# Optimization experiments

Measured on AMD Instinct MI355X. Metric: run time of the kernel, lower is better.

Reference implementation:

```python
import jax, jax.numpy as jnp
import numpy as np

B, C, RN, K = 4, 128, 4096, 16
EPS = 1e-5

def _bn_relu(x, gamma, beta):
    # BatchNorm1d in training mode: batch stats over axis 0 (biased var)
    mu = jnp.mean(x, axis=0)
    var = jnp.mean(jnp.square(x - mu), axis=0)
    y = (x - mu) / jnp.sqrt(var + EPS) * gamma + beta
    return jax.nn.relu(y)

def _mlp(x, W, b, gamma, beta):
    return _bn_relu(x @ W.T + b, gamma, beta)

def _knn_idx(pts, k):
    # pts: (B, N, 3) -> (B, N, k) indices of k nearest (incl. self)
    sq = jnp.sum(pts * pts, axis=-1)  # (B, N)
    d2 = sq[:, :, None] + sq[:, None, :] - 2.0 * jnp.einsum('bnd,bmd->bnm', pts, pts)
    _, idx = jax.lax.top_k(-d2, k)
    return idx

def _group(feats, idx):
    # feats: (B, N, C), idx: (B, N, k) -> (B, N, k, C)
    return jax.vmap(lambda f, i: f[i])(feats, idx)

def setup_inputs() -> dict:
    key = jax.random.key(0)
    ks = jax.random.split(key, 16)
    def init_lin(k1, k2, out_c, in_c):
        lim = 1.0 / np.sqrt(in_c)
        W = jax.random.uniform(k1, (out_c, in_c), jnp.float32, -lim, lim)
        b = jax.random.uniform(k2, (out_c,), jnp.float32, -lim, lim)
        return W, b
    W1, b1 = init_lin(ks[0], ks[1], 64, 3)
    W2, b2 = init_lin(ks[2], ks[3], C, C + 64)
    Ww, bw = init_lin(ks[4], ks[5], K, 3)
    return {
        'F_E': jax.random.normal(ks[6], (B, C, RN), jnp.float32),
        'Q_prime': jax.random.normal(ks[7], (B, 3, RN), jnp.float32),
        'W1': W1, 'b1': b1, 'g1': jnp.ones((64,), jnp.float32), 'be1': jnp.zeros((64,), jnp.float32),
        'W2': W2, 'b2': b2, 'g2': jnp.ones((C,), jnp.float32), 'be2': jnp.zeros((C,), jnp.float32),
        'Ww': Ww, 'bw': bw, 'gw': jnp.ones((K,), jnp.float32), 'bew': jnp.zeros((K,), jnp.float32),
    }

def reference(F_E, Q_prime, W1, b1, g1, be1, W2, b2, g2, be2, Ww, bw, gw, bew):
    q = jnp.transpose(Q_prime, (0, 2, 1))   # (B, rN, 3)
    f = jnp.transpose(F_E, (0, 2, 1))       # (B, rN, C)
    idx = _knn_idx(q, K)                     # (B, rN, K)
    grouped_Q = _group(q, idx)               # (B, rN, K, 3)
    grouped_F = _group(f, idx)               # (B, rN, K, C)
    sub_Q = grouped_Q - q[:, :, None, :]     # (B, rN, K, 3)
    sub_flat = sub_Q.reshape(-1, 3)
    enc_sub = _mlp(sub_flat, W1, b1, g1, be1).reshape(B, RN, K, 64)
    concat = jnp.concatenate([grouped_F, enc_sub], axis=-1).reshape(-1, C + 64)
    enc_feat = _mlp(concat, W2, b2, g2, be2).reshape(B, RN, K, C)
    sw = _mlp(sub_flat, Ww, bw, gw, bew).reshape(B, RN, K, K)
    # einsum 'brkc,brkk->brkc' takes the diagonal of sw over its last two axes
    w_diag = jnp.diagonal(sw, axis1=2, axis2=3)  # (B, rN, K)
    weighted = jnp.sum(enc_feat * w_diag[..., None], axis=2)  # (B, rN, C)
    refined = weighted + f
    return jnp.transpose(refined, (0, 2, 1))
```

## Files before the change

kernel.cpp:

```cpp
#include <hip/hip_runtime.h>
#include <hip/hip_bf16.h>

#define BB 4
#define CC 128
#define RN 4096
#define KK 16
#define NROWS (BB*RN*KK)
#define EPSV 1e-5f

typedef __attribute__((ext_vector_type(8))) short short8;
typedef __attribute__((ext_vector_type(4))) float f32x4;

__device__ inline ushort f2bf(float f) {
    union { __hip_bfloat16 h; ushort u; } cv;
    cv.h = __float2bfloat16(f);
    return cv.u;
}

__device__ inline float readlane_f(float v, int src) {
    return __uint_as_float((uint)__builtin_amdgcn_readlane((int)__float_as_uint(v), src));
}


__global__ void k_prep(const float* __restrict__ Q, float4* __restrict__ qp,
                       const float* __restrict__ W2, ushort* __restrict__ W2b) {
    int blk = blockIdx.x;
    if (blk < 64) {
        int gid = blk * 256 + threadIdx.x;
        int b = gid >> 12, n = gid & (RN - 1);
        size_t base = (size_t)b * 3 * RN;
        float x = Q[base + n], y = Q[base + RN + n], z = Q[base + 2 * RN + n];
        qp[gid] = make_float4(x, y, z, fmaf(x, x, fmaf(y, y, z * z)));
    } else {
        int i = (blk - 64) * 256 + threadIdx.x;
        if (i < 128 * 192) W2b[i] = f2bf(W2[i]);
    }
}

__global__ void k_transpose(const float* __restrict__ FE, ushort* __restrict__ ftb) {
    __shared__ float t[32][33];
    int bid = blockIdx.x;
    int b = bid >> 9;
    int cb = (bid >> 7) & 3;
    int nb = bid & 127;
    int c0 = cb * 32, n0 = nb * 32;
    int tid = threadIdx.x;
    for (int o = tid; o < 1024; o += 256) {
        int i = o >> 5, j = o & 31;
        t[i][j] = FE[((size_t)b * CC + c0 + i) * RN + n0 + j];
    }
    __syncthreads();
    for (int o = tid; o < 512; o += 256) {
        int j = o >> 4, i2 = (o & 15) * 2;
        uint p = (uint)f2bf(t[i2][j]) | ((uint)f2bf(t[i2 + 1][j]) << 16);
        *(uint*)(ftb + ((size_t)(b * RN + n0 + j) * 128 + c0 + i2)) = p;
    }
}

__global__ __launch_bounds__(256) void k_knn(const float4* __restrict__ qp, int* __restrict__ idxout,
                                             float* __restrict__ zwout, float* __restrict__ statslots,
                                             const float* __restrict__ Ww, const float* __restrict__ bw) {
    __shared__ float bacc[9];
    const int tid = threadIdx.x;
    if (tid < 9) bacc[tid] = 0.f;
    __syncthreads();
    const int lane = tid & 63;
    const int wid = tid >> 6;
    const int row = blockIdx.x * 4 + wid;
    const int b = row >> 12, n = row & (RN - 1);
    const float4* qb = qp + b * RN;
    const float4 self = qb[n];
    const int upaddr = ((lane - 1) & 63) << 2;

    float ld; int li;
    {
        float4 cp = qb[lane];
        ld = self.w + cp.w - 2.f * fmaf(self.x, cp.x, fmaf(self.y, cp.y, self.z * cp.z));
        li = lane;
        #pragma unroll
        for (int k = 2; k <= 64; k <<= 1) {
            #pragma unroll
            for (int j = k >> 1; j > 0; j >>= 1) {
                float od = __shfl_xor(ld, j);
                int   oi = __shfl_xor(li, j);
                bool up    = ((lane & k) == 0);
                bool lower = ((lane & j) == 0);
                bool myless = (ld < od) || (ld == od && li < oi);
                bool keep = (myless == lower) == up;
                if (!keep) { ld = od; li = oi; }
            }
        }
    }
    float g15d = readlane_f(ld, 15);
    int   g15i = __builtin_amdgcn_readlane(li, 15);

    float4 cur = qb[64 + lane];
    for (int t0 = 64; t0 < RN; t0 += 64) {
        float4 nxt = qb[t0 + 64 + lane];
        const float d2 = self.w + cur.w - 2.f * fmaf(self.x, cur.x, fmaf(self.y, cur.y, self.z * cur.z));
        bool beats = (d2 < g15d) || (d2 == g15d && (t0 + lane) < g15i);
        unsigned long long mask = __ballot(beats);
        if (mask) {
            do {
                float sd = __uint_as_float((uint)__builtin_amdgcn_ds_bpermute(upaddr, (int)__float_as_uint(ld)));
                int   si = __builtin_amdgcn_ds_bpermute(upaddr, li);
                int src = (int)__builtin_ctzll(mask);
                mask &= mask - 1;
                float cd = readlane_f(d2, src);
                int   ci = t0 + src;
                bool lt2 = (ld < cd) || (ld == cd && li < ci);
                int p = (int)__builtin_popcountll(__ballot(lt2) & 0xFFFFull);
                if (lane == p)      { ld = cd; li = ci; }
                else if (lane > p)  { ld = sd; li = si; }
            } while (mask);
            g15d = readlane_f(ld, 15);
            g15i = __builtin_amdgcn_readlane(li, 15);
        }
        cur = nxt;
    }

    float sx = 0.f, sy = 0.f, sz = 0.f;
    if (lane < 16) {
        idxout[row * 16 + lane] = li;
        float4 pn = qb[li];
        sx = pn.x - self.x; sy = pn.y - self.y; sz = pn.z - self.z;
        float zw = fmaf(Ww[lane * 3], sx, fmaf(Ww[lane * 3 + 1], sy, fmaf(Ww[lane * 3 + 2], sz, bw[lane])));
        zwout[row * 16 + lane] = zw;
    }
    float vals[9] = {sx, sy, sz, sx * sx, sx * sy, sx * sz, sy * sy, sy * sz, sz * sz};
    #pragma unroll
    for (int i = 0; i < 9; ++i) {
        float v = vals[i];
        for (int off = 32; off; off >>= 1) v += __shfl_down(v, off);
        if (lane == 0) atomicAdd(&bacc[i], v);
    }
    __syncthreads();
    if (tid < 9) atomicAdd(&statslots[(blockIdx.x & 63) * 12 + tid], bacc[tid]);
}

__global__ void k_bn1(const float* __restrict__ slots, const float* __restrict__ W1, const float* __restrict__ b1,
                      const float* __restrict__ g1, const float* __restrict__ be1,
                      const float* __restrict__ Ww, const float* __restrict__ bw,
                      const float* __restrict__ gw, const float* __restrict__ bew, float* __restrict__ par) {
    __shared__ float st[12];
    int tid = threadIdx.x;
    if (tid < 12) {
        float s = 0.f;
        for (int i = 0; i < 64; ++i) s += slots[i * 12 + tid];
        st[tid] = s;
    }
    __syncthreads();
    const float invN = 1.0f / (float)NROWS;
    float mx = st[0] * invN, my = st[1] * invN, mz = st[2] * invN;
    float Cxx = st[3] * invN - mx * mx, Cxy = st[4] * invN - mx * my, Cxz = st[5] * invN - mx * mz;
    float Cyy = st[6] * invN - my * my, Cyz = st[7] * invN - my * mz, Czz = st[8] * invN - mz * mz;
    if (tid < 64) {
        float w0 = W1[tid * 3], w1 = W1[tid * 3 + 1], w2 = W1[tid * 3 + 2];
        float mean = w0 * mx + w1 * my + w2 * mz + b1[tid];
        float var = w0 * w0 * Cxx + w1 * w1 * Cyy + w2 * w2 * Czz
                  + 2.f * (w0 * w1 * Cxy + w0 * w2 * Cxz + w1 * w2 * Cyz);
        float sc = g1[tid] * rsqrtf(var + EPSV);
        par[tid] = sc;
        par[64 + tid] = be1[tid] - mean * sc;
    } else if (tid < 80) {
        int k = tid - 64;
        float w0 = Ww[k * 3], w1 = Ww[k * 3 + 1], w2 = Ww[k * 3 + 2];
        float mean = w0 * mx + w1 * my + w2 * mz + bw[k];
        float var = w0 * w0 * Cxx + w1 * w1 * Cyy + w2 * w2 * Czz
                  + 2.f * (w0 * w1 * Cxy + w0 * w2 * Cxz + w1 * w2 * Cyz);
        float sc = gw[k] * rsqrtf(var + EPSV);
        par[128 + k] = sc;
        par[144 + k] = bew[k] - mean * sc;
    }
}

__global__ __launch_bounds__(256) void k_main(const ushort* __restrict__ ftb, const int* __restrict__ idxb,
                                              const float4* __restrict__ qp, const float* __restrict__ W1,
                                              const float* __restrict__ b1, const ushort* __restrict__ W2b,
                                              const float* __restrict__ b2, const float* __restrict__ par,
                                              float* __restrict__ bn2slots, __hip_bfloat16* __restrict__ z2) {
    __shared__ ushort enc_lds[64][72];
    __shared__ float subs[64][3];
    __shared__ int nbr[64];
    const int tid = threadIdx.x;
    const int bid = blockIdx.x;
    const int pair0 = bid * 4;
    const int b = pair0 >> 12;

    if (tid < 64) {
        int g = tid >> 4, k = tid & 15;
        int pair = pair0 + g;
        int n = idxb[pair * 16 + k];
        nbr[tid] = n;
        float4 pn = qp[b * RN + n];
        float4 ps = qp[pair];
        subs[tid][0] = pn.x - ps.x;
        subs[tid][1] = pn.y - ps.y;
        subs[tid][2] = pn.z - ps.z;
    }
    __syncthreads();
    for (int o = tid; o < 2048; o += 256) {
        int r = o >> 5, c2 = (o & 31) * 2;
        float z0 = fmaf(W1[c2 * 3],     subs[r][0], fmaf(W1[c2 * 3 + 1], subs[r][1], fmaf(W1[c2 * 3 + 2], subs[r][2], b1[c2])));
        float z1 = fmaf(W1[c2 * 3 + 3], subs[r][0], fmaf(W1[c2 * 3 + 4], subs[r][1], fmaf(W1[c2 * 3 + 5], subs[r][2], b1[c2 + 1])));
        float e0 = fmaxf(fmaf(z0, par[c2],     par[64 + c2]),     0.f);
        float e1 = fmaxf(fmaf(z1, par[c2 + 1], par[64 + c2 + 1]), 0.f);
        *(uint*)&enc_lds[r][c2] = (uint)f2bf(e0) | ((uint)f2bf(e1) << 16);
    }
    __syncthreads();

    const int lane = tid & 63, w = tid >> 6;
    const int lr = lane & 15, lg = lane >> 4;
    const int cbase = w * 32;

    short8 af[12];
    #pragma unroll
    for (int ct = 0; ct < 2; ++ct)
        #pragma unroll
        for (int kt = 0; kt < 6; ++kt)
            af[ct * 6 + kt] = *(const short8*)(W2b + (size_t)(cbase + ct * 16 + lr) * 192 + kt * 32 + lg * 8);

    float4 b2v[2];
    b2v[0] = *(const float4*)&b2[cbase + lg * 4];
    b2v[1] = *(const float4*)&b2[cbase + 16 + lg * 4];

    float st_s[8], st_q[8];
    #pragma unroll
    for (int i = 0; i < 8; ++i) { st_s[i] = 0.f; st_q[i] = 0.f; }

    #pragma unroll
    for (int nt = 0; nt < 4; ++nt) {
        const int r = nt * 16 + lr;
        const ushort* fr = ftb + ((size_t)(b * RN + nbr[r]) * 128) + lg * 8;
        short8 bf[6];
        bf[0] = *(const short8*)(fr);
        bf[1] = *(const short8*)(fr + 32);
        bf[2] = *(const short8*)(fr + 64);
        bf[3] = *(const short8*)(fr + 96);
        bf[4] = *(const short8*)&enc_lds[r][lg * 8];
        bf[5] = *(const short8*)&enc_lds[r][32 + lg * 8];
        #pragma unroll
        for (int ct = 0; ct < 2; ++ct) {
            f32x4 acc = {0.f, 0.f, 0.f, 0.f};
            #pragma unroll
            for (int kt = 0; kt < 6; ++kt)
                acc = __builtin_amdgcn_mfma_f32_16x16x32_bf16(af[ct * 6 + kt], bf[kt], acc, 0, 0, 0);
            const int c0 = cbase + ct * 16 + lg * 4;
            const size_t row = (size_t)pair0 * 16 + nt * 16 + lr;
            union { __hip_bfloat16 h[4]; uint2 u2; } pk;
            const float4 bb = b2v[ct];
            float vb[4] = {bb.x, bb.y, bb.z, bb.w};
            #pragma unroll
            for (int cc = 0; cc < 4; ++cc) {
                float v = acc[cc] + vb[cc];
                st_s[ct * 4 + cc] += v;
                st_q[ct * 4 + cc] = fmaf(v, v, st_q[ct * 4 + cc]);
                pk.h[cc] = __float2bfloat16(v);
            }
            *(uint2*)(z2 + row * CC + c0) = pk.u2;
        }
    }
    #pragma unroll
    for (int i = 0; i < 8; ++i) {
        float s = st_s[i], q = st_q[i];
        #pragma unroll
        for (int m = 1; m < 16; m <<= 1) { s += __shfl_xor(s, m); q += __shfl_xor(q, m); }
        if (lr == 0) {
            int ct = i >> 2, cc = i & 3;
            int c = cbase + ct * 16 + lg * 4 + cc;
            atomicAdd(&bn2slots[(bid & 63) * 256 + c * 2], s);
            atomicAdd(&bn2slots[(bid & 63) * 256 + c * 2 + 1], q);
        }
    }
}

__global__ void k_bn2(const float* __restrict__ slots, const float* __restrict__ g2,
                      const float* __restrict__ be2, float* __restrict__ par) {
    __shared__ float red[256];
    int tid = threadIdx.x;
    float v = 0.f;
    for (int s = 0; s < 64; ++s) v += slots[s * 256 + tid];
    red[tid] = v;
    __syncthreads();
    if (tid < 128) {
        const float invN = 1.0f / (float)NROWS;
        float mean = red[2 * tid] * invN;
        float var = red[2 * tid + 1] * invN - mean * mean;
        float sc = g2[tid] * rsqrtf(var + EPSV);
        par[160 + tid] = sc;
        par[288 + tid] = be2[tid] - mean * sc;
    }
}

__global__ __launch_bounds__(256) void k_out(const __hip_bfloat16* __restrict__ z2, const float* __restrict__ zw_raw,
                                             const float* __restrict__ par, const float* __restrict__ F_E,
                                             float* __restrict__ out) {
    __shared__ float wd[32][16];
    __shared__ float outs[32][129];
    const int tid = threadIdx.x;
    const int b = blockIdx.x >> 7;
    const int r0 = (blockIdx.x & 127) * 32;
    const int rowbase = (b * RN + r0) * 16;
    for (int o = tid; o < 512; o += 256) {
        int rr = o >> 4, k = o & 15;
        wd[rr][k] = fmaxf(fmaf(zw_raw[rowbase + o], par[128 + k], par[144 + k]), 0.f);
    }
    __syncthreads();
    const int c0 = (tid & 63) * 2;
    const int rh = tid >> 6;
    const float sc0 = par[160 + c0], sh0 = par[288 + c0];
    const float sc1 = par[160 + c0 + 1], sh1 = par[288 + c0 + 1];
    for (int rr = rh; rr < 32; rr += 4) {
        float a0 = 0.f, a1 = 0.f;
        const __hip_bfloat16* zp = z2 + ((size_t)rowbase + rr * 16) * CC + c0;
        #pragma unroll
        for (int k = 0; k < 16; ++k) {
            unsigned int uu = *(const unsigned int*)(zp + k * CC);
            float z0 = __uint_as_float(uu << 16);
            float z1 = __uint_as_float(uu & 0xFFFF0000u);
            float w = wd[rr][k];
            a0 += fmaxf(fmaf(z0, sc0, sh0), 0.f) * w;
            a1 += fmaxf(fmaf(z1, sc1, sh1), 0.f) * w;
        }
        outs[rr][c0] = a0; outs[rr][c0 + 1] = a1;
    }
    __syncthreads();
    for (int o = tid; o < 4096; o += 256) {
        int c = o >> 5, rr = o & 31;
        size_t oi = ((size_t)b * CC + c) * RN + r0 + rr;
        out[oi] = outs[rr][c] + F_E[oi];
    }
}

extern "C" void kernel_launch(void* const* d_in, const int* in_sizes, int n_in,
                              void* d_out, int out_size, void* d_ws, size_t ws_size,
                              hipStream_t stream) {
    const float* F_E = (const float*)d_in[0];
    const float* Qp  = (const float*)d_in[1];
    const float* W1  = (const float*)d_in[2];
    const float* b1  = (const float*)d_in[3];
    const float* g1  = (const float*)d_in[4];
    const float* be1 = (const float*)d_in[5];
    const float* W2  = (const float*)d_in[6];
    const float* b2  = (const float*)d_in[7];
    const float* g2  = (const float*)d_in[8];
    const float* be2 = (const float*)d_in[9];
    const float* Ww  = (const float*)d_in[10];
    const float* bw  = (const float*)d_in[11];
    const float* gw  = (const float*)d_in[12];
    const float* bew = (const float*)d_in[13];
    float* out = (float*)d_out;
    float* wsf = (float*)d_ws;

    float* bn2slots   = wsf;
    float* statslots  = wsf + 16384;
    float* par        = wsf + 17152;
    ushort* W2b       = (ushort*)(wsf + 17664);
    float4* qpack     = (float4*)(wsf + 32768);
    int* idxb         = (int*)(wsf + 98304);
    float* zw_raw     = wsf + 360448;
    ushort* ftb       = (ushort*)(wsf + 622592);
    __hip_bfloat16* z2 = (__hip_bfloat16*)(wsf + 1671168);

    hipMemsetAsync(d_ws, 0, 17152 * sizeof(float), stream);
    k_prep<<<160, 256, 0, stream>>>(Qp, qpack, W2, W2b);
    k_transpose<<<2048, 256, 0, stream>>>(F_E, ftb);
    k_knn<<<4096, 256, 0, stream>>>(qpack, idxb, zw_raw, statslots, Ww, bw);
    k_bn1<<<1, 128, 0, stream>>>(statslots, W1, b1, g1, be1, Ww, bw, gw, bew, par);
    k_main<<<4096, 256, 0, stream>>>(ftb, idxb, qpack, W1, b1, W2b, b2, par, bn2slots, z2);
    k_bn2<<<1, 256, 0, stream>>>(bn2slots, g2, be2, par);
    k_out<<<512, 256, 0, stream>>>(z2, zw_raw, par, F_E, out);
}
```

Measured before the change: 270.9 us.

## Recompute second GEMM in fused output kernel instead of materializing z2

After: 328.7 us. 21.3% more time.

```diff
diff --git a/kernel.cpp b/kernel.cpp
--- a/kernel.cpp
+++ b/kernel.cpp
@@ -174,11 +174,11 @@
     }
 }
 
-__global__ __launch_bounds__(256) void k_main(const ushort* __restrict__ ftb, const int* __restrict__ idxb,
-                                              const float4* __restrict__ qp, const float* __restrict__ W1,
-                                              const float* __restrict__ b1, const ushort* __restrict__ W2b,
-                                              const float* __restrict__ b2, const float* __restrict__ par,
-                                              float* __restrict__ bn2slots, __hip_bfloat16* __restrict__ z2) {
+__global__ __launch_bounds__(256, 4) void k_stats(const ushort* __restrict__ ftb, const int* __restrict__ idxb,
+                                                  const float4* __restrict__ qp, const float* __restrict__ W1,
+                                                  const float* __restrict__ b1, const ushort* __restrict__ W2b,
+                                                  const float* __restrict__ b2, const float* __restrict__ par,
+                                                  float* __restrict__ bn2slots) {
     __shared__ ushort enc_lds[64][72];
     __shared__ float subs[64][3];
     __shared__ int nbr[64];
@@ -245,9 +245,6 @@
             #pragma unroll
             for (int kt = 0; kt < 6; ++kt)
                 acc = __builtin_amdgcn_mfma_f32_16x16x32_bf16(af[ct * 6 + kt], bf[kt], acc, 0, 0, 0);
-            const int c0 = cbase + ct * 16 + lg * 4;
-            const size_t row = (size_t)pair0 * 16 + nt * 16 + lr;
-            union { __hip_bfloat16 h[4]; uint2 u2; } pk;
             const float4 bb = b2v[ct];
             float vb[4] = {bb.x, bb.y, bb.z, bb.w};
             #pragma unroll
@@ -255,9 +252,7 @@
                 float v = acc[cc] + vb[cc];
                 st_s[ct * 4 + cc] += v;
                 st_q[ct * 4 + cc] = fmaf(v, v, st_q[ct * 4 + cc]);
-                pk.h[cc] = __float2bfloat16(v);
             }
-            *(uint2*)(z2 + row * CC + c0) = pk.u2;
         }
     }
     #pragma unroll
@@ -292,43 +287,112 @@
     }
 }
 
-__global__ __launch_bounds__(256) void k_out(const __hip_bfloat16* __restrict__ z2, const float* __restrict__ zw_raw,
-                                             const float* __restrict__ par, const float* __restrict__ F_E,
-                                             float* __restrict__ out) {
-    __shared__ float wd[32][16];
-    __shared__ float outs[32][129];
+__global__ __launch_bounds__(256, 4) void k_fuse(const ushort* __restrict__ ftb, const int* __restrict__ idxb,
+                                                 const float4* __restrict__ qp, const float* __restrict__ W1,
+                                                 const float* __restrict__ b1, const ushort* __restrict__ W2b,
+                                                 const float* __restrict__ b2, const float* __restrict__ par,
+                                                 const float* __restrict__ zw_raw, const float* __restrict__ F_E,
+                                                 float* __restrict__ out) {
+    __shared__ ushort enc_lds[64][72];
+    __shared__ float subs[64][3];
+    __shared__ int nbr[64];
+    __shared__ float outs[128][4];
     const int tid = threadIdx.x;
-    const int b = blockIdx.x >> 7;
-    const int r0 = (blockIdx.x & 127) * 32;
-    const int rowbase = (b * RN + r0) * 16;
-    for (int o = tid; o < 512; o += 256) {
-        int rr = o >> 4, k = o & 15;
-        wd[rr][k] = fmaxf(fmaf(zw_raw[rowbase + o], par[128 + k], par[144 + k]), 0.f);
-    }
-    __syncthreads();
-    const int c0 = (tid & 63) * 2;
-    const int rh = tid >> 6;
-    const float sc0 = par[160 + c0], sh0 = par[288 + c0];
-    const float sc1 = par[160 + c0 + 1], sh1 = par[288 + c0 + 1];
-    for (int rr = rh; rr < 32; rr += 4) {
-        float a0 = 0.f, a1 = 0.f;
-        const __hip_bfloat16* zp = z2 + ((size_t)rowbase + rr * 16) * CC + c0;
-        #pragma unroll
-        for (int k = 0; k < 16; ++k) {
-            unsigned int uu = *(const unsigned int*)(zp + k * CC);
-            float z0 = __uint_as_float(uu << 16);
-            float z1 = __uint_as_float(uu & 0xFFFF0000u);
-            float w = wd[rr][k];
-            a0 += fmaxf(fmaf(z0, sc0, sh0), 0.f) * w;
-            a1 += fmaxf(fmaf(z1, sc1, sh1), 0.f) * w;
+    const int bid = blockIdx.x;
+    const int pair0 = bid * 4;
+    const int b = pair0 >> 12;
+    const int n0 = pair0 & (RN - 1);
+
+    if (tid < 64) {
+        int g = tid >> 4, k = tid & 15;
+        int pair = pair0 + g;
+        int n = idxb[pair * 16 + k];
+        nbr[tid] = n;
+        float4 pn = qp[b * RN + n];
+        float4 ps = qp[pair];
+        subs[tid][0] = pn.x - ps.x;
+        subs[tid][1] = pn.y - ps.y;
+        subs[tid][2] = pn.z - ps.z;
+    }
+    __syncthreads();
+    for (int o = tid; o < 2048; o += 256) {
+        int r = o >> 5, c2 = (o & 31) * 2;
+        float z0 = fmaf(W1[c2 * 3],     subs[r][0], fmaf(W1[c2 * 3 + 1], subs[r][1], fmaf(W1[c2 * 3 + 2], subs[r][2], b1[c2])));
+        float z1 = fmaf(W1[c2 * 3 + 3], subs[r][0], fmaf(W1[c2 * 3 + 4], subs[r][1], fmaf(W1[c2 * 3 + 5], subs[r][2], b1[c2 + 1])));
+        float e0 = fmaxf(fmaf(z0, par[c2],     par[64 + c2]),     0.f);
+        float e1 = fmaxf(fmaf(z1, par[c2 + 1], par[64 + c2 + 1]), 0.f);
+        *(uint*)&enc_lds[r][c2] = (uint)f2bf(e0) | ((uint)f2bf(e1) << 16);
+    }
+    __syncthreads();
+
+    const int lane = tid & 63, w = tid >> 6;
+    const int lr = lane & 15, lg = lane >> 4;
+    const int cbase = w * 32;
+
+    short8 af[12];
+    #pragma unroll
+    for (int ct = 0; ct < 2; ++ct)
+        #pragma unroll
+        for (int kt = 0; kt < 6; ++kt)
+            af[ct * 6 + kt] = *(const short8*)(W2b + (size_t)(cbase + ct * 16 + lr) * 192 + kt * 32 + lg * 8);
+
+    float4 b2v[2], s2v[2], h2v[2];
+    b2v[0] = *(const float4*)&b2[cbase + lg * 4];
+    b2v[1] = *(const float4*)&b2[cbase + 16 + lg * 4];
+    s2v[0] = *(const float4*)&par[160 + cbase + lg * 4];
+    s2v[1] = *(const float4*)&par[160 + cbase + 16 + lg * 4];
+    h2v[0] = *(const float4*)&par[288 + cbase + lg * 4];
+    h2v[1] = *(const float4*)&par[288 + cbase + 16 + lg * 4];
+    const float scw = par[128 + lr], shw = par[144 + lr];
+
+    #pragma unroll
+    for (int nt = 0; nt < 4; ++nt) {
+        const int r = nt * 16 + lr;
+        const ushort* fr = ftb + ((size_t)(b * RN + nbr[r]) * 128) + lg * 8;
+        short8 bf[6];
+        bf[0] = *(const short8*)(fr);
+        bf[1] = *(const short8*)(fr + 32);
+        bf[2] = *(const short8*)(fr + 64);
+        bf[3] = *(const short8*)(fr + 96);
+        bf[4] = *(const short8*)&enc_lds[r][lg * 8];
+        bf[5] = *(const short8*)&enc_lds[r][32 + lg * 8];
+        const float wdv = fmaxf(fmaf(zw_raw[(size_t)(pair0 + nt) * 16 + lr], scw, shw), 0.f);
+        #pragma unroll
+        for (int ct = 0; ct < 2; ++ct) {
+            f32x4 acc = {0.f, 0.f, 0.f, 0.f};
+            #pragma unroll
+            for (int kt = 0; kt < 6; ++kt)
+                acc = __builtin_amdgcn_mfma_f32_16x16x32_bf16(af[ct * 6 + kt], bf[kt], acc, 0, 0, 0);
+            const float4 bb = b2v[ct];
+            const float4 ss = s2v[ct];
+            const float4 hh = h2v[ct];
+            float vb[4] = {bb.x, bb.y, bb.z, bb.w};
+            float vs[4] = {ss.x, ss.y, ss.z, ss.w};
+            float vh[4] = {hh.x, hh.y, hh.z, hh.w};
+            float y[4];
+            #pragma unroll
+            for (int cc = 0; cc < 4; ++cc) {
+                float v = acc[cc] + vb[cc];
+                y[cc] = fmaxf(fmaf(v, vs[cc], vh[cc]), 0.f) * wdv;
+            }
+            #pragma unroll
+            for (int m = 1; m < 16; m <<= 1) {
+                #pragma unroll
+                for (int cc = 0; cc < 4; ++cc) y[cc] += __shfl_xor(y[cc], m);
+            }
+            if (lr == 0) {
+                const int c0 = cbase + ct * 16 + lg * 4;
+                #pragma unroll
+                for (int cc = 0; cc < 4; ++cc) outs[c0 + cc][nt] = y[cc];
+            }
         }
-        outs[rr][c0] = a0; outs[rr][c0 + 1] = a1;
-    }
-    __syncthreads();
-    for (int o = tid; o < 4096; o += 256) {
-        int c = o >> 5, rr = o & 31;
-        size_t oi = ((size_t)b * CC + c) * RN + r0 + rr;
-        out[oi] = outs[rr][c] + F_E[oi];
+    }
+    __syncthreads();
+    if (tid < 128) {
+        size_t base = ((size_t)b * CC + tid) * RN + n0;
+        float4 o4 = *(float4*)&outs[tid][0];
+        float4 fe4 = *(const float4*)&F_E[base];
+        *(float4*)&out[base] = make_float4(o4.x + fe4.x, o4.y + fe4.y, o4.z + fe4.z, o4.w + fe4.w);
     }
 }
 
@@ -360,14 +424,13 @@
     int* idxb         = (int*)(wsf + 98304);
     float* zw_raw     = wsf + 360448;
     ushort* ftb       = (ushort*)(wsf + 622592);
-    __hip_bfloat16* z2 = (__hip_bfloat16*)(wsf + 1671168);
 
     hipMemsetAsync(d_ws, 0, 17152 * sizeof(float), stream);
     k_prep<<<160, 256, 0, stream>>>(Qp, qpack, W2, W2b);
     k_transpose<<<2048, 256, 0, stream>>>(F_E, ftb);
     k_knn<<<4096, 256, 0, stream>>>(qpack, idxb, zw_raw, statslots, Ww, bw);
     k_bn1<<<1, 128, 0, stream>>>(statslots, W1, b1, g1, be1, Ww, bw, gw, bew, par);
-    k_main<<<4096, 256, 0, stream>>>(ftb, idxb, qpack, W1, b1, W2b, b2, par, bn2slots, z2);
+    k_stats<<<4096, 256, 0, stream>>>(ftb, idxb, qpack, W1, b1, W2b, b2, par, bn2slots);
     k_bn2<<<1, 256, 0, stream>>>(bn2slots, g2, be2, par);
-    k_out<<<512, 256, 0, stream>>>(z2, zw_raw, par, F_E, out);
-}
+    k_fuse<<<4096, 256, 0, stream>>>(ftb, idxb, qpack, W1, b1, W2b, b2, par, zw_raw, F_E, out);
+}
```

## Software-pipeline neighbor feature gathers and remap blocks in k_main

Applied to the files above, without the earlier changes.

Result: no change. 268.3 us (-1.0%).

```diff
diff --git a/kernel.cpp b/kernel.cpp
--- a/kernel.cpp
+++ b/kernel.cpp
@@ -174,31 +174,42 @@
     }
 }
 
-__global__ __launch_bounds__(256) void k_main(const ushort* __restrict__ ftb, const int* __restrict__ idxb,
-                                              const float4* __restrict__ qp, const float* __restrict__ W1,
-                                              const float* __restrict__ b1, const ushort* __restrict__ W2b,
-                                              const float* __restrict__ b2, const float* __restrict__ par,
-                                              float* __restrict__ bn2slots, __hip_bfloat16* __restrict__ z2) {
+__global__ __launch_bounds__(256, 3) void k_main(const ushort* __restrict__ ftb, const int* __restrict__ idxb,
+                                                 const float4* __restrict__ qp, const float* __restrict__ W1,
+                                                 const float* __restrict__ b1, const ushort* __restrict__ W2b,
+                                                 const float* __restrict__ b2, const float* __restrict__ par,
+                                                 float* __restrict__ bn2slots, __hip_bfloat16* __restrict__ z2) {
     __shared__ ushort enc_lds[64][72];
     __shared__ float subs[64][3];
     __shared__ int nbr[64];
     const int tid = threadIdx.x;
-    const int bid = blockIdx.x;
-    const int pair0 = bid * 4;
+    const int tile = ((blockIdx.x & 7) << 9) | (blockIdx.x >> 3);
+    const int pair0 = tile * 4;
     const int b = pair0 >> 12;
-
-    if (tid < 64) {
-        int g = tid >> 4, k = tid & 15;
-        int pair = pair0 + g;
-        int n = idxb[pair * 16 + k];
-        nbr[tid] = n;
+    const int lane = tid & 63, w = tid >> 6;
+    const int lr = lane & 15, lg = lane >> 4;
+
+    if (lane < 16) {
+        int pair = pair0 + w;
+        int n = idxb[pair * 16 + lane];
+        int r = w * 16 + lane;
+        nbr[r] = n;
         float4 pn = qp[b * RN + n];
         float4 ps = qp[pair];
-        subs[tid][0] = pn.x - ps.x;
-        subs[tid][1] = pn.y - ps.y;
-        subs[tid][2] = pn.z - ps.z;
-    }
-    __syncthreads();
+        subs[r][0] = pn.x - ps.x;
+        subs[r][1] = pn.y - ps.y;
+        subs[r][2] = pn.z - ps.z;
+    }
+    __syncthreads();
+
+    const int cbase = w * 32;
+    short8 af[12];
+    #pragma unroll
+    for (int ct = 0; ct < 2; ++ct)
+        #pragma unroll
+        for (int kt = 0; kt < 6; ++kt)
+            af[ct * 6 + kt] = *(const short8*)(W2b + (size_t)(cbase + ct * 16 + lr) * 192 + kt * 32 + lg * 8);
+
     for (int o = tid; o < 2048; o += 256) {
         int r = o >> 5, c2 = (o & 31) * 2;
         float z0 = fmaf(W1[c2 * 3],     subs[r][0], fmaf(W1[c2 * 3 + 1], subs[r][1], fmaf(W1[c2 * 3 + 2], subs[r][2], b1[c2])));
@@ -209,17 +220,6 @@
     }
     __syncthreads();
 
-    const int lane = tid & 63, w = tid >> 6;
-    const int lr = lane & 15, lg = lane >> 4;
-    const int cbase = w * 32;
-
-    short8 af[12];
-    #pragma unroll
-    for (int ct = 0; ct < 2; ++ct)
-        #pragma unroll
-        for (int kt = 0; kt < 6; ++kt)
-            af[ct * 6 + kt] = *(const short8*)(W2b + (size_t)(cbase + ct * 16 + lr) * 192 + kt * 32 + lg * 8);
-
     float4 b2v[2];
     b2v[0] = *(const float4*)&b2[cbase + lg * 4];
     b2v[1] = *(const float4*)&b2[cbase + 16 + lg * 4];
@@ -228,25 +228,36 @@
     #pragma unroll
     for (int i = 0; i < 8; ++i) { st_s[i] = 0.f; st_q[i] = 0.f; }
 
-    #pragma unroll
+    const ushort* fr0 = ftb + ((size_t)(b * RN + nbr[lr]) * 128) + lg * 8;
+    short8 c0_ = *(const short8*)(fr0);
+    short8 c1_ = *(const short8*)(fr0 + 32);
+    short8 c2_ = *(const short8*)(fr0 + 64);
+    short8 c3_ = *(const short8*)(fr0 + 96);
+
+    #pragma unroll 1
     for (int nt = 0; nt < 4; ++nt) {
+        short8 n0_ = c0_, n1_ = c1_, n2_ = c2_, n3_ = c3_;
+        if (nt < 3) {
+            const ushort* fr = ftb + ((size_t)(b * RN + nbr[(nt + 1) * 16 + lr]) * 128) + lg * 8;
+            n0_ = *(const short8*)(fr);
+            n1_ = *(const short8*)(fr + 32);
+            n2_ = *(const short8*)(fr + 64);
+            n3_ = *(const short8*)(fr + 96);
+        }
         const int r = nt * 16 + lr;
-        const ushort* fr = ftb + ((size_t)(b * RN + nbr[r]) * 128) + lg * 8;
-        short8 bf[6];
-        bf[0] = *(const short8*)(fr);
-        bf[1] = *(const short8*)(fr + 32);
-        bf[2] = *(const short8*)(fr + 64);
-        bf[3] = *(const short8*)(fr + 96);
-        bf[4] = *(const short8*)&enc_lds[r][lg * 8];
-        bf[5] = *(const short8*)&enc_lds[r][32 + lg * 8];
+        short8 be0 = *(const short8*)&enc_lds[r][lg * 8];
+        short8 be1 = *(const short8*)&enc_lds[r][32 + lg * 8];
+        const size_t row = (size_t)pair0 * 16 + r;
         #pragma unroll
         for (int ct = 0; ct < 2; ++ct) {
             f32x4 acc = {0.f, 0.f, 0.f, 0.f};
-            #pragma unroll
-            for (int kt = 0; kt < 6; ++kt)
-                acc = __builtin_amdgcn_mfma_f32_16x16x32_bf16(af[ct * 6 + kt], bf[kt], acc, 0, 0, 0);
-            const int c0 = cbase + ct * 16 + lg * 4;
-            const size_t row = (size_t)pair0 * 16 + nt * 16 + lr;
+            acc = __builtin_amdgcn_mfma_f32_16x16x32_bf16(af[ct * 6 + 0], c0_, acc, 0, 0, 0);
+            acc = __builtin_amdgcn_mfma_f32_16x16x32_bf16(af[ct * 6 + 1], c1_, acc, 0, 0, 0);
+            acc = __builtin_amdgcn_mfma_f32_16x16x32_bf16(af[ct * 6 + 2], c2_, acc, 0, 0, 0);
+            acc = __builtin_amdgcn_mfma_f32_16x16x32_bf16(af[ct * 6 + 3], c3_, acc, 0, 0, 0);
+            acc = __builtin_amdgcn_mfma_f32_16x16x32_bf16(af[ct * 6 + 4], be0, acc, 0, 0, 0);
+            acc = __builtin_amdgcn_mfma_f32_16x16x32_bf16(af[ct * 6 + 5], be1, acc, 0, 0, 0);
+            const int c0ch = cbase + ct * 16 + lg * 4;
             union { __hip_bfloat16 h[4]; uint2 u2; } pk;
             const float4 bb = b2v[ct];
             float vb[4] = {bb.x, bb.y, bb.z, bb.w};
@@ -257,8 +268,9 @@
                 st_q[ct * 4 + cc] = fmaf(v, v, st_q[ct * 4 + cc]);
                 pk.h[cc] = __float2bfloat16(v);
             }
-            *(uint2*)(z2 + row * CC + c0) = pk.u2;
-        }
+            *(uint2*)(z2 + row * CC + c0ch) = pk.u2;
+        }
+        c0_ = n0_; c1_ = n1_; c2_ = n2_; c3_ = n3_;
     }
     #pragma unroll
     for (int i = 0; i < 8; ++i) {
@@ -268,8 +280,8 @@
         if (lr == 0) {
             int ct = i >> 2, cc = i & 3;
             int c = cbase + ct * 16 + lg * 4 + cc;
-            atomicAdd(&bn2slots[(bid & 63) * 256 + c * 2], s);
-            atomicAdd(&bn2slots[(bid & 63) * 256 + c * 2 + 1], q);
+            atomicAdd(&bn2slots[(tile & 63) * 256 + c * 2], s);
+            atomicAdd(&bn2slots[(tile & 63) * 256 + c * 2 + 1], q);
         }
     }
 }
```
